# Performance work log

Measured on AMD Instinct MI355X. Metric: run time of the kernel, lower is better.

The kernel has to match this reference:

```python
import jax, jax.numpy as jnp
import numpy as np

NEG_SLOPE = 0.2  # PyG GATConv default leaky_relu slope


def gat_conv(x, ei, W, a_src, a_dst, b, heads, ch):
    """One PyG-style GATConv (eval mode, add_self_loops already applied to ei)."""
    N = x.shape[0]
    h = (x @ W).reshape(N, heads, ch)                      # [N,H,C]
    src, dst = ei[0], ei[1]
    al_s = jnp.sum(h * a_src, axis=-1)                     # [N,H]
    al_d = jnp.sum(h * a_dst, axis=-1)                     # [N,H]
    e = jax.nn.leaky_relu(al_s[src] + al_d[dst], NEG_SLOPE)  # [E,H]
    m = jax.ops.segment_max(e, dst, num_segments=N)        # stable softmax over in-edges
    ex = jnp.exp(e - m[dst])
    den = jax.ops.segment_sum(ex, dst, num_segments=N)
    alpha = ex / den[dst]                                  # [E,H]
    msg = alpha[:, :, None] * h[src]                       # [E,H,C]
    out = jax.ops.segment_sum(msg, dst, num_segments=N)    # [N,H,C]
    return out.reshape(N, heads * ch) + b


def setup_inputs() -> dict:
    key = jax.random.key(0)
    ks = jax.random.split(key, 12)
    N, E, D_in, C, H, D_out = 10000, 320000, 256, 128, 4, 64
    HC = H * C

    def glorot(k, shape):
        fan = shape[0] + shape[-1]
        return jax.random.normal(k, shape, dtype=jnp.float32) * np.sqrt(2.0 / fan)

    x = jax.random.normal(ks[0], (N, D_in), dtype=jnp.float32)
    edge_index = jax.random.randint(ks[1], (2, E), 0, N, dtype=jnp.int64)
    return {
        "x": x,
        "edge_index": edge_index,
        "W1": glorot(ks[2], (D_in, HC)),
        "a_src1": glorot(ks[3], (H, C)),
        "a_dst1": glorot(ks[4], (H, C)),
        "b1": jnp.zeros((HC,), dtype=jnp.float32),
        "W2": glorot(ks[5], (HC, HC)),
        "a_src2": glorot(ks[6], (H, C)),
        "a_dst2": glorot(ks[7], (H, C)),
        "b2": jnp.zeros((HC,), dtype=jnp.float32),
        "W3": glorot(ks[8], (HC, D_out)),
        "a_src3": glorot(ks[9], (1, D_out)),
        "a_dst3": glorot(ks[10], (1, D_out)),
        "b3": jnp.zeros((D_out,), dtype=jnp.float32),
    }


def reference(x, edge_index, W1, a_src1, a_dst1, b1, W2, a_src2, a_dst2, b2,
              W3, a_src3, a_dst3, b3):
    N = x.shape[0]
    loops = jnp.arange(N, dtype=edge_index.dtype)
    ei = jnp.concatenate([edge_index, jnp.stack([loops, loops])], axis=1)
    H, C = a_src1.shape
    h = jax.nn.elu(gat_conv(x, ei, W1, a_src1, a_dst1, b1, H, C))
    h = jax.nn.elu(gat_conv(h, ei, W2, a_src2, a_dst2, b2, H, C))
    out = gat_conv(h, ei, W3, a_src3, a_dst3, b3, 1, a_src3.shape[1])
    return out
```

## Files before the change

kernel.cpp:

```cpp
#include <hip/hip_runtime.h>
#include <hip/hip_fp16.h>

typedef _Float16 f16x8 __attribute__((ext_vector_type(8)));
typedef float f32x4 __attribute__((ext_vector_type(4)));

__device__ __forceinline__ unsigned short f2h_bits(float f) {
    __half h = __float2half(f);
    return *reinterpret_cast<unsigned short*>(&h);
}
__device__ __forceinline__ float h2f_bits(unsigned short u) {
    __half h = *reinterpret_cast<__half*>(&u);
    return __half2float(h);
}

__device__ __forceinline__ void fma_mix_lo(float& acc, float a, unsigned hw) {
    asm("v_fma_mix_f32 %0, %1, %2, %0 op_sel_hi:[0,1,0]"
        : "+v"(acc) : "v"(a), "v"(hw));
}
__device__ __forceinline__ void fma_mix_hi(float& acc, float a, unsigned hw) {
    asm("v_fma_mix_f32 %0, %1, %2, %0 op_sel:[0,1,0] op_sel_hi:[0,1,0]"
        : "+v"(acc) : "v"(a), "v"(hw));
}

__device__ __forceinline__ float elu_fast(float v) {
    float e = __expf(v) - 1.f;
    return v > 0.f ? v : e;
}

__device__ __forceinline__ void gload_lds16(const void* g, void* l) {
    __builtin_amdgcn_global_load_lds(
        (const __attribute__((address_space(1))) unsigned int*)g,
        (__attribute__((address_space(3))) unsigned int*)l, 16, 0, 0);
}

__global__ void k_prep(const float* __restrict__ W1, unsigned short* __restrict__ W1T,
                       const float* __restrict__ W2, unsigned short* __restrict__ W2T,
                       const float* __restrict__ W3, unsigned short* __restrict__ W3T,
                       const float* __restrict__ x, unsigned short* __restrict__ xb,
                       int* __restrict__ csr, int Mcap,
                       const int* __restrict__ ei, int E, int* __restrict__ deg,
                       int DIN, int HC, int DOUT, int N)
{
    int i = blockIdx.x * blockDim.x + threadIdx.x;
    int n1 = DIN * HC;
    int n2 = n1 + HC * HC;
    int n3 = n2 + HC * DOUT;
    int n4 = n3 + N * DIN;
    int n5 = n4 + Mcap;
    int n6 = n5 + E;
    if (i < n1) {
        int k = i / HC, n = i - k * HC;
        W1T[n * DIN + k] = f2h_bits(W1[i]);
    } else if (i < n2) {
        int j = i - n1;
        int k = j / HC, n = j - k * HC;
        W2T[n * HC + k] = f2h_bits(W2[j]);
    } else if (i < n3) {
        int j = i - n2;
        int k = j / DOUT, n = j - k * DOUT;
        W3T[n * HC + k] = f2h_bits(W3[j]);
    } else if (i < n4) {
        int j = i - n3;
        xb[j] = f2h_bits(x[j]);
    } else if (i < n5) {
        csr[i - n4] = -1;
    } else if (i < n6) {
        atomicAdd(&deg[ei[E + (i - n5)]], 1);
    }
}

__global__ void k_scan(const int* __restrict__ deg, int* __restrict__ off,
                       int* __restrict__ cur, int N) {
    __shared__ int sums[1024];
    int t = threadIdx.x;
    int chunk = (N + 1023) >> 10;
    int lo = t * chunk;
    int hi = lo + chunk; if (hi > N) hi = N;
    if (lo > N) lo = N;
    int s = 0;
    for (int i = lo; i < hi; ++i) s += (deg[i] + 4) & ~3;
    sums[t] = s;
    __syncthreads();
    for (int dd = 1; dd < 1024; dd <<= 1) {
        int v = (t >= dd) ? sums[t - dd] : 0;
        __syncthreads();
        sums[t] += v;
        __syncthreads();
    }
    int run = sums[t] - s;
    for (int i = lo; i < hi; ++i) { off[i] = run; cur[i] = run; run += (deg[i] + 4) & ~3; }
    if (t == 1023) off[N] = run;
}
__global__ void k_fill(const int* __restrict__ ei, int E, int N,
                       int* cur, int* __restrict__ csr) {
    int i = blockIdx.x * blockDim.x + threadIdx.x;
    if (i < E) {
        int s = ei[i], d = ei[E + i];
        int pos = atomicAdd(&cur[d], 1);
        csr[pos] = s;
    } else if (i < E + N) {
        int nn = i - E;
        int pos = atomicAdd(&cur[nn], 1);
        csr[pos] = nn;
    }
}

template <bool OUTH, bool DOAL>
__global__ __launch_bounds__(256) void k_gemm(
    const unsigned short* __restrict__ A, const unsigned short* __restrict__ BT,
    void* __restrict__ D, int M, int K, int Nc, int tiles_n,
    const float* __restrict__ asrc, const float* __restrict__ adst,
    float* __restrict__ als, float* __restrict__ ald)
{
    int wid = blockIdx.x * (blockDim.x >> 6) + (threadIdx.x >> 6);
    int tiles_m = (M + 63) >> 6;
    if (wid >= tiles_m * tiles_n) return;
    int lane = threadIdx.x & 63;
    int tm = wid / tiles_n, tn = wid - tm * tiles_n;
    int m0 = tm << 6, n0 = tn << 6;
    int r = lane & 15, q = lane >> 4;

    const unsigned short* Arow[4];
    const unsigned short* Brow[4];
#pragma unroll
    for (int i = 0; i < 4; ++i) {
        int row = m0 + 16 * i + r; row = row < M ? row : M - 1;
        Arow[i] = A + (size_t)row * K + q * 8;
        Brow[i] = BT + (size_t)(n0 + 16 * i + r) * K + q * 8;
    }

    f32x4 acc[4][4] = {};
    f16x8 a[4], b[4], a2[4], b2[4];
#pragma unroll
    for (int i = 0; i < 4; ++i) {
        a[i] = *(const f16x8*)(Arow[i]);
        b[i] = *(const f16x8*)(Brow[i]);
    }
    for (int k0 = 0; k0 < K; k0 += 32) {
        int kn = k0 + 32;
        if (kn < K) {
#pragma unroll
            for (int i = 0; i < 4; ++i) {
                a2[i] = *(const f16x8*)(Arow[i] + kn);
                b2[i] = *(const f16x8*)(Brow[i] + kn);
            }
        }
#pragma unroll
        for (int i = 0; i < 4; ++i)
#pragma unroll
            for (int j = 0; j < 4; ++j)
                acc[i][j] = __builtin_amdgcn_mfma_f32_16x16x32_f16(a[i], b[j], acc[i][j], 0, 0, 0);
        if (kn < K) {
#pragma unroll
            for (int i = 0; i < 4; ++i) { a[i] = a2[i]; b[i] = b2[i]; }
        }
    }
#pragma unroll
    for (int i = 0; i < 4; ++i) {
        int rowb = m0 + 16 * i + q * 4;
#pragma unroll
        for (int rr = 0; rr < 4; ++rr) {
            int row = rowb + rr;
            if (row < M) {
#pragma unroll
                for (int j = 0; j < 4; ++j) {
                    int col = n0 + 16 * j + r;
                    if (OUTH)
                        ((unsigned short*)D)[(size_t)row * Nc + col] = f2h_bits(acc[i][j][rr]);
                    else
                        ((float*)D)[(size_t)row * Nc + col] = acc[i][j][rr];
                }
            }
        }
    }
    if (DOAL) {
        float asl[4], adl[4];
#pragma unroll
        for (int j = 0; j < 4; ++j) { asl[j] = asrc[16 * j + r]; adl[j] = adst[16 * j + r]; }
#pragma unroll
        for (int i = 0; i < 4; ++i) {
#pragma unroll
            for (int rr = 0; rr < 4; ++rr) {
                float s = 0.f, d = 0.f;
#pragma unroll
                for (int j = 0; j < 4; ++j) {
                    s += acc[i][j][rr] * asl[j];
                    d += acc[i][j][rr] * adl[j];
                }
#pragma unroll
                for (int dd = 1; dd < 16; dd <<= 1) {
                    s += __shfl_xor(s, dd);
                    d += __shfl_xor(d, dd);
                }
                int row = m0 + 16 * i + q * 4 + rr;
                if (r == 0 && row < M) { als[row] = s; ald[row] = d; }
            }
        }
    }
}

__global__ __launch_bounds__(256) void k_gemm_lds(
    const unsigned short* __restrict__ A, const unsigned short* __restrict__ BT,
    unsigned short* __restrict__ D, int M, int K, int Nc, int tiles_n)
{
    __shared__ unsigned short As[128 * 32];
    __shared__ unsigned short Bs[64 * 32];
    int tm = blockIdx.x / tiles_n, tn = blockIdx.x - tm * tiles_n;
    int m0 = tm << 7, n0 = tn << 6;
    int tid = threadIdx.x;
    int w = tid >> 6, lane = tid & 63;
    int wr = w >> 1, wc = w & 1;
    int r = lane & 15, q = lane >> 4;

    int lrow = lane >> 2;
    int lch = (lane & 3) * 8;
    int ga0 = m0 + w * 16 + lrow;       if (ga0 >= M) ga0 = M - 1;
    int ga1 = m0 + (w + 4) * 16 + lrow; if (ga1 >= M) ga1 = M - 1;
    const unsigned short* pa0 = A + (size_t)ga0 * K + lch;
    const unsigned short* pa1 = A + (size_t)ga1 * K + lch;
    const unsigned short* pb  = BT + (size_t)(n0 + w * 16 + lrow) * K + lch;
    unsigned short* lA0 = As + w * 512;
    unsigned short* lA1 = As + (w + 4) * 512;
    unsigned short* lB  = Bs + w * 512;

    const unsigned short* arp = As + (wr * 64 + r) * 32 + q * 8;
    const unsigned short* brp = Bs + (wc * 32 + r) * 32 + q * 8;

    f32x4 acc[4][2] = {};
    for (int k0 = 0; k0 < K; k0 += 32) {
        gload_lds16(pa0 + k0, lA0);
        gload_lds16(pa1 + k0, lA1);
        gload_lds16(pb + k0, lB);
        __syncthreads();
        f16x8 a[4], b[2];
#pragma unroll
        for (int i = 0; i < 4; ++i) a[i] = *(const f16x8*)(arp + i * 16 * 32);
#pragma unroll
        for (int j = 0; j < 2; ++j) b[j] = *(const f16x8*)(brp + j * 16 * 32);
#pragma unroll
        for (int i = 0; i < 4; ++i)
#pragma unroll
            for (int j = 0; j < 2; ++j)
                acc[i][j] = __builtin_amdgcn_mfma_f32_16x16x32_f16(a[i], b[j], acc[i][j], 0, 0, 0);
        __syncthreads();
    }
#pragma unroll
    for (int i = 0; i < 4; ++i) {
        int rowb = m0 + wr * 64 + 16 * i + q * 4;
#pragma unroll
        for (int rr = 0; rr < 4; ++rr) {
            int row = rowb + rr;
            if (row < M) {
#pragma unroll
                for (int j = 0; j < 2; ++j) {
                    int col = n0 + wc * 32 + 16 * j + r;
                    D[(size_t)row * Nc + col] = f2h_bits(acc[i][j][rr]);
                }
            }
        }
    }
}

template <int HCt, int Ht>
__global__ __launch_bounds__(256) void k_al(
    const unsigned short* __restrict__ h, const float* __restrict__ asrc,
    const float* __restrict__ adst,
    float* __restrict__ als, float* __restrict__ ald, int N)
{
    int wid = blockIdx.x * (blockDim.x >> 6) + (threadIdx.x >> 6);
    if (wid >= N) return;
    int lane = threadIdx.x & 63;
    const int CH = HCt / 64;
    const int Gs = 64 / Ht;
    float s = 0.f, d = 0.f;
    if constexpr (CH == 8) {
        const uint4* hr = (const uint4*)(h + (size_t)wid * HCt) + lane;
        uint4 hv = *hr;
        unsigned wds[4] = {hv.x, hv.y, hv.z, hv.w};
        const f32x4* as4 = (const f32x4*)(asrc + lane * 8);
        const f32x4* ad4 = (const f32x4*)(adst + lane * 8);
        f32x4 av0 = as4[0], av1 = as4[1], dv0 = ad4[0], dv1 = ad4[1];
#pragma unroll
        for (int wv = 0; wv < 4; ++wv) {
            float a0 = (wv < 2) ? av0[2 * wv] : av1[2 * (wv - 2)];
            float a1 = (wv < 2) ? av0[2 * wv + 1] : av1[2 * (wv - 2) + 1];
            float d0 = (wv < 2) ? dv0[2 * wv] : dv1[2 * (wv - 2)];
            float d1 = (wv < 2) ? dv0[2 * wv + 1] : dv1[2 * (wv - 2) + 1];
            fma_mix_lo(s, a0, wds[wv]); fma_mix_hi(s, a1, wds[wv]);
            fma_mix_lo(d, d0, wds[wv]); fma_mix_hi(d, d1, wds[wv]);
        }
    } else {
        float hv = h2f_bits(h[(size_t)wid * HCt + lane]);
        s = hv * asrc[lane];
        d = hv * adst[lane];
    }
#pragma unroll
    for (int dd = 1; dd < Gs; dd <<= 1) {
        s += __shfl_xor(s, dd);
        d += __shfl_xor(d, dd);
    }
    if ((lane & (Gs - 1)) == 0) {
        int hh = lane / Gs;
        als[wid * Ht + hh] = s;
        ald[wid * Ht + hh] = d;
    }
}

template <bool DOELU>
__global__ __launch_bounds__(256) void k_aggr4f(
    const unsigned short* __restrict__ h, const float* __restrict__ als,
    const float* __restrict__ ald,
    const int* __restrict__ off, const int* __restrict__ csr,
    const float* __restrict__ bias,
    unsigned short* __restrict__ outp, int N, int nodeBlocks)
{
    __shared__ float alpS[4][64];
    __shared__ int   csrS[4][64];
    int head = blockIdx.x / nodeBlocks;
    int nb = blockIdx.x - head * nodeBlocks;
    int wid = threadIdx.x >> 6;
    int n = nb * 4 + wid;
    if (n >= N) return;
    int lane = threadIdx.x & 63;
    int g = lane >> 4;
    int p = lane & 15;

    int off0 = off[n];
    int degp = off[n + 1] - off0;
    float aldh = ald[n * 4 + head];
    const char* hB = (const char*)h;
    const unsigned offp = (unsigned)(head * 256 + p * 16);

    float acc[8] = {};
    float den = 0.f;

    for (int base = 0; base < degp; base += 64) {
        float av = 0.f;
        int sc = 0;
        int e = base + lane;
        if (e < degp) {
            int s = csr[off0 + e];
            if (s >= 0) {
                sc = s;
                float l = als[(size_t)(unsigned)s * 4 + head] + aldh;
                l = l > 0.f ? l : 0.2f * l;
                av = __expf(l);
            }
        }
        alpS[wid][lane] = av;
        csrS[wid][lane] = sc;

        int qn = (degp - base) >> 2; if (qn > 16) qn = 16;
        for (int qq = g; qq < qn; qq += 4) {
            int4 cs = *(const int4*)&csrS[wid][qq * 4];
            f32x4 af = *(const f32x4*)&alpS[wid][qq * 4];
            uint4 h0 = *(const uint4*)(hB + (size_t)((((unsigned)cs.x) << 10) + offp));
            uint4 h1 = *(const uint4*)(hB + (size_t)((((unsigned)cs.y) << 10) + offp));
            uint4 h2 = *(const uint4*)(hB + (size_t)((((unsigned)cs.z) << 10) + offp));
            uint4 h3 = *(const uint4*)(hB + (size_t)((((unsigned)cs.w) << 10) + offp));
            den += (af[0] + af[1]) + (af[2] + af[3]);
            unsigned w0[4] = {h0.x, h0.y, h0.z, h0.w};
            unsigned w1[4] = {h1.x, h1.y, h1.z, h1.w};
            unsigned w2[4] = {h2.x, h2.y, h2.z, h2.w};
            unsigned w3[4] = {h3.x, h3.y, h3.z, h3.w};
#pragma unroll
            for (int wv = 0; wv < 4; ++wv) {
                fma_mix_lo(acc[2 * wv],     af[0], w0[wv]);
                fma_mix_hi(acc[2 * wv + 1], af[0], w0[wv]);
            }
#pragma unroll
            for (int wv = 0; wv < 4; ++wv) {
                fma_mix_lo(acc[2 * wv],     af[1], w1[wv]);
                fma_mix_hi(acc[2 * wv + 1], af[1], w1[wv]);
            }
#pragma unroll
            for (int wv = 0; wv < 4; ++wv) {
                fma_mix_lo(acc[2 * wv],     af[2], w2[wv]);
                fma_mix_hi(acc[2 * wv + 1], af[2], w2[wv]);
            }
#pragma unroll
            for (int wv = 0; wv < 4; ++wv) {
                fma_mix_lo(acc[2 * wv],     af[3], w3[wv]);
                fma_mix_hi(acc[2 * wv + 1], af[3], w3[wv]);
            }
        }
    }

    den += __shfl_xor(den, 16);
    den += __shfl_xor(den, 32);
#pragma unroll
    for (int j = 0; j < 8; ++j) {
        acc[j] += __shfl_xor(acc[j], 16);
        acc[j] += __shfl_xor(acc[j], 32);
    }

    if (g == 0) {
        float inv = 1.f / den;
        int cb = head * 128 + p * 8;
        unsigned ww[4];
#pragma unroll
        for (int wv = 0; wv < 4; ++wv) {
            float v0 = acc[2 * wv] * inv + bias[cb + 2 * wv];
            float v1 = acc[2 * wv + 1] * inv + bias[cb + 2 * wv + 1];
            if (DOELU) {
                v0 = elu_fast(v0);
                v1 = elu_fast(v1);
            }
            ww[wv] = (unsigned)f2h_bits(v0) | ((unsigned)f2h_bits(v1) << 16);
        }
        uint4 o; o.x = ww[0]; o.y = ww[1]; o.z = ww[2]; o.w = ww[3];
        *((uint4*)(outp + (size_t)n * 512 + cb)) = o;
    }
}

__global__ __launch_bounds__(256) void k_aggr1c(
    const unsigned short* __restrict__ h, const float* __restrict__ als,
    const float* __restrict__ aldv, const int* __restrict__ off,
    const int* __restrict__ csr, const float* __restrict__ bias,
    float* __restrict__ outp, int N)
{
    __shared__ float alpS[4][64];
    __shared__ int   csrS[4][64];
    int wid = threadIdx.x >> 6;
    int n = blockIdx.x * 4 + wid;
    if (n >= N) return;
    int lane = threadIdx.x & 63;
    int g = lane >> 4;
    int p = lane & 15;

    int off0 = off[n];
    int degp = off[n + 1] - off0;
    float aldh = aldv[n];
    const char* hB = (const char*)h;
    const unsigned offp = (unsigned)(p * 8);

    float acc[4] = {};
    float den = 0.f;

    for (int base = 0; base < degp; base += 64) {
        float av = 0.f;
        int sc = 0;
        int e = base + lane;
        if (e < degp) {
            int s = csr[off0 + e];
            if (s >= 0) {
                sc = s;
                float l = als[s] + aldh;
                l = l > 0.f ? l : 0.2f * l;
                av = __expf(l);
            }
        }
        alpS[wid][lane] = av;
        csrS[wid][lane] = sc;

        int qn = (degp - base) >> 2; if (qn > 16) qn = 16;
        for (int qq = g; qq < qn; qq += 4) {
            int4 cs = *(const int4*)&csrS[wid][qq * 4];
            f32x4 af = *(const f32x4*)&alpS[wid][qq * 4];
            uint2 h0 = *(const uint2*)(hB + (size_t)((((unsigned)cs.x) << 7) + offp));
            uint2 h1 = *(const uint2*)(hB + (size_t)((((unsigned)cs.y) << 7) + offp));
            uint2 h2 = *(const uint2*)(hB + (size_t)((((unsigned)cs.z) << 7) + offp));
            uint2 h3 = *(const uint2*)(hB + (size_t)((((unsigned)cs.w) << 7) + offp));
            den += (af[0] + af[1]) + (af[2] + af[3]);
            fma_mix_lo(acc[0], af[0], h0.x);
            fma_mix_hi(acc[1], af[0], h0.x);
            fma_mix_lo(acc[2], af[0], h0.y);
            fma_mix_hi(acc[3], af[0], h0.y);
            fma_mix_lo(acc[0], af[1], h1.x);
            fma_mix_hi(acc[1], af[1], h1.x);
            fma_mix_lo(acc[2], af[1], h1.y);
            fma_mix_hi(acc[3], af[1], h1.y);
            fma_mix_lo(acc[0], af[2], h2.x);
            fma_mix_hi(acc[1], af[2], h2.x);
            fma_mix_lo(acc[2], af[2], h2.y);
            fma_mix_hi(acc[3], af[2], h2.y);
            fma_mix_lo(acc[0], af[3], h3.x);
            fma_mix_hi(acc[1], af[3], h3.x);
            fma_mix_lo(acc[2], af[3], h3.y);
            fma_mix_hi(acc[3], af[3], h3.y);
        }
    }

    den += __shfl_xor(den, 16);
    den += __shfl_xor(den, 32);
#pragma unroll
    for (int j = 0; j < 4; ++j) {
        acc[j] += __shfl_xor(acc[j], 16);
        acc[j] += __shfl_xor(acc[j], 32);
    }
    if (g == 0) {
        float inv = 1.f / den;
        f32x4 o;
#pragma unroll
        for (int j = 0; j < 4; ++j)
            o[j] = acc[j] * inv + bias[p * 4 + j];
        *((f32x4*)(outp + (size_t)n * 64 + p * 4)) = o;
    }
}

extern "C" void kernel_launch(void* const* d_in, const int* in_sizes, int n_in,
                              void* d_out, int out_size, void* d_ws, size_t ws_size,
                              hipStream_t stream)
{
    const float* x   = (const float*)d_in[0];
    const int*   ei  = (const int*)d_in[1];
    const float* W1  = (const float*)d_in[2];
    const float* as1 = (const float*)d_in[3];
    const float* ad1 = (const float*)d_in[4];
    const float* b1  = (const float*)d_in[5];
    const float* W2  = (const float*)d_in[6];
    const float* as2 = (const float*)d_in[7];
    const float* ad2 = (const float*)d_in[8];
    const float* b2  = (const float*)d_in[9];
    const float* W3  = (const float*)d_in[10];
    const float* as3 = (const float*)d_in[11];
    const float* ad3 = (const float*)d_in[12];
    const float* b3  = (const float*)d_in[13];

    const int DIN = 256, HC = 512, DOUT = 64;
    int N = in_sizes[0] / DIN;
    int E = in_sizes[1] / 2;
    int Mcap = E + 4 * N;

    char* w = (char*)d_ws;
    auto alloc = [&](size_t bytes) -> char* {
        char* p = w;
        w += (bytes + 255) & ~(size_t)255;
        return p;
    };
    int* deg    = (int*)alloc((size_t)N * 4);
    int* cur    = (int*)alloc((size_t)N * 4);
    int* off    = (int*)alloc((size_t)(N + 1) * 4);
    int* csr    = (int*)alloc((size_t)Mcap * 4);
    unsigned short* W1T = (unsigned short*)alloc((size_t)HC * DIN * 2);
    unsigned short* W2T = (unsigned short*)alloc((size_t)HC * HC * 2);
    unsigned short* W3T = (unsigned short*)alloc((size_t)DOUT * HC * 2);
    unsigned short* xb  = (unsigned short*)alloc((size_t)N * DIN * 2);
    unsigned short* act = (unsigned short*)alloc((size_t)N * HC * 2);
    unsigned short* hb  = (unsigned short*)alloc((size_t)N * HC * 2);
    unsigned short* hb3 = (unsigned short*)alloc((size_t)N * DOUT * 2);
    float* als   = (float*)alloc((size_t)N * 4 * 4);
    float* ald   = (float*)alloc((size_t)N * 4 * 4);

    hipMemsetAsync(deg, 0, (size_t)N * 4, stream);
    int prep_total = DIN * HC + HC * HC + HC * DOUT + N * DIN + Mcap + E;
    k_prep<<<(prep_total + 255) / 256, 256, 0, stream>>>(
        W1, W1T, W2, W2T, W3, W3T, x, xb, csr, Mcap, ei, E, deg, DIN, HC, DOUT, N);
    k_scan<<<1, 1024, 0, stream>>>(deg, off, cur, N);
    k_fill<<<(E + N + 255) / 256, 256, 0, stream>>>(ei, E, N, cur, csr);

    int tiles_m = (N + 63) / 64;
    auto gemm_blocks = [&](int tn) { return (tiles_m * tn + 3) / 4; };
    int tm128 = (N + 127) / 128;
    int nwave_blocks = (N + 3) / 4;
    int nodeBlocks = (N + 3) / 4;

    k_gemm_lds<<<tm128 * (HC / 64), 256, 0, stream>>>(xb, W1T, hb, N, DIN, HC, HC / 64);
    k_al<512, 4><<<nwave_blocks, 256, 0, stream>>>(hb, as1, ad1, als, ald, N);
    k_aggr4f<true><<<4 * nodeBlocks, 256, 0, stream>>>(hb, als, ald, off, csr, b1, act, N, nodeBlocks);

    k_gemm_lds<<<tm128 * (HC / 64), 256, 0, stream>>>(act, W2T, hb, N, HC, HC, HC / 64);
    k_al<512, 4><<<nwave_blocks, 256, 0, stream>>>(hb, as2, ad2, als, ald, N);
    k_aggr4f<true><<<4 * nodeBlocks, 256, 0, stream>>>(hb, als, ald, off, csr, b2, act, N, nodeBlocks);

    k_gemm<true, true><<<gemm_blocks(1), 256, 0, stream>>>(
        act, W3T, hb3, N, HC, DOUT, 1, as3, ad3, als, ald);
    k_aggr1c<<<nwave_blocks, 256, 0, stream>>>(hb3, als, ald, off, csr, b3, (float*)d_out, N);
}
```

Before: 263.8 us.

## Fold attention vectors into extra GEMM columns and drop k_al kernels

Precomputes W·a_src and W·a_dst per head as eight extra columns appended to the transposed fp16 weights (padded to 64 columns). The GEMM gets one extra column tile whose accumulators are written directly as the attention logits, so the separate k_al kernel, which re-read the whole hidden matrix, is removed for layers 1 and 2. The cost is an extra tile of MMA work per row block, a few more prep threads, and logits computed from fp16-rounded folded weights rather than from rounded h, which changes numerics slightly.

```diff
diff --git a/kernel.cpp b/kernel.cpp
--- a/kernel.cpp
+++ b/kernel.cpp
@@ -39,6 +39,8 @@
                        const float* __restrict__ x, unsigned short* __restrict__ xb,
                        int* __restrict__ csr, int Mcap,
                        const int* __restrict__ ei, int E, int* __restrict__ deg,
+                       const float* __restrict__ as1, const float* __restrict__ ad1,
+                       const float* __restrict__ as2, const float* __restrict__ ad2,
                        int DIN, int HC, int DOUT, int N)
 {
     int i = blockIdx.x * blockDim.x + threadIdx.x;
@@ -48,6 +50,9 @@
     int n4 = n3 + N * DIN;
     int n5 = n4 + Mcap;
     int n6 = n5 + E;
+    int n7 = n6 + 8 * DIN;
+    int n8 = n7 + 8 * HC;
+    int n9 = n8 + 56 * DIN + 56 * HC;
     if (i < n1) {
         int k = i / HC, n = i - k * HC;
         W1T[n * DIN + k] = f2h_bits(W1[i]);
@@ -66,6 +71,28 @@
         csr[i - n4] = -1;
     } else if (i < n6) {
         atomicAdd(&deg[ei[E + (i - n5)]], 1);
+    } else if (i < n7) {
+        int j = i - n6;
+        int h8 = j / DIN, k = j - h8 * DIN;
+        int hh = h8 & 3;
+        const float* av = (h8 < 4 ? as1 : ad1) + hh * 128;
+        const float* wr = W1 + (size_t)k * HC + hh * 128;
+        float s = 0.f;
+        for (int c = 0; c < 128; ++c) s += wr[c] * av[c];
+        W1T[(size_t)(HC + h8) * DIN + k] = f2h_bits(s);
+    } else if (i < n8) {
+        int j = i - n7;
+        int h8 = j / HC, k = j - h8 * HC;
+        int hh = h8 & 3;
+        const float* av = (h8 < 4 ? as2 : ad2) + hh * 128;
+        const float* wr = W2 + (size_t)k * HC + hh * 128;
+        float s = 0.f;
+        for (int c = 0; c < 128; ++c) s += wr[c] * av[c];
+        W2T[(size_t)(HC + h8) * HC + k] = f2h_bits(s);
+    } else if (i < n9) {
+        int j = i - n8;
+        if (j < 56 * DIN) W1T[(size_t)(HC + 8) * DIN + j] = 0;
+        else              W2T[(size_t)(HC + 8) * HC + (j - 56 * DIN)] = 0;
     }
 }
 
@@ -201,7 +228,8 @@
 
 __global__ __launch_bounds__(256) void k_gemm_lds(
     const unsigned short* __restrict__ A, const unsigned short* __restrict__ BT,
-    unsigned short* __restrict__ D, int M, int K, int Nc, int tiles_n)
+    unsigned short* __restrict__ D, int M, int K, int Nc, int tiles_n,
+    float* __restrict__ als, float* __restrict__ ald)
 {
     __shared__ unsigned short As[128 * 32];
     __shared__ unsigned short Bs[64 * 32];
@@ -244,6 +272,20 @@
                 acc[i][j] = __builtin_amdgcn_mfma_f32_16x16x32_f16(a[i], b[j], acc[i][j], 0, 0, 0);
         __syncthreads();
     }
+    if (tn == tiles_n - 1) {
+        if (wc == 0 && r < 8) {
+            float* dst = (r < 4) ? als : ald;
+            int hh = r & 3;
+#pragma unroll
+            for (int i = 0; i < 4; ++i)
+#pragma unroll
+                for (int rr = 0; rr < 4; ++rr) {
+                    int row = m0 + wr * 64 + 16 * i + q * 4 + rr;
+                    if (row < M) dst[row * 4 + hh] = acc[i][0][rr];
+                }
+        }
+        return;
+    }
 #pragma unroll
     for (int i = 0; i < 4; ++i) {
         int rowb = m0 + wr * 64 + 16 * i + q * 4;
@@ -258,51 +300,6 @@
                 }
             }
         }
-    }
-}
-
-template <int HCt, int Ht>
-__global__ __launch_bounds__(256) void k_al(
-    const unsigned short* __restrict__ h, const float* __restrict__ asrc,
-    const float* __restrict__ adst,
-    float* __restrict__ als, float* __restrict__ ald, int N)
-{
-    int wid = blockIdx.x * (blockDim.x >> 6) + (threadIdx.x >> 6);
-    if (wid >= N) return;
-    int lane = threadIdx.x & 63;
-    const int CH = HCt / 64;
-    const int Gs = 64 / Ht;
-    float s = 0.f, d = 0.f;
-    if constexpr (CH == 8) {
-        const uint4* hr = (const uint4*)(h + (size_t)wid * HCt) + lane;
-        uint4 hv = *hr;
-        unsigned wds[4] = {hv.x, hv.y, hv.z, hv.w};
-        const f32x4* as4 = (const f32x4*)(asrc + lane * 8);
-        const f32x4* ad4 = (const f32x4*)(adst + lane * 8);
-        f32x4 av0 = as4[0], av1 = as4[1], dv0 = ad4[0], dv1 = ad4[1];
-#pragma unroll
-        for (int wv = 0; wv < 4; ++wv) {
-            float a0 = (wv < 2) ? av0[2 * wv] : av1[2 * (wv - 2)];
-            float a1 = (wv < 2) ? av0[2 * wv + 1] : av1[2 * (wv - 2) + 1];
-            float d0 = (wv < 2) ? dv0[2 * wv] : dv1[2 * (wv - 2)];
-            float d1 = (wv < 2) ? dv0[2 * wv + 1] : dv1[2 * (wv - 2) + 1];
-            fma_mix_lo(s, a0, wds[wv]); fma_mix_hi(s, a1, wds[wv]);
-            fma_mix_lo(d, d0, wds[wv]); fma_mix_hi(d, d1, wds[wv]);
-        }
-    } else {
-        float hv = h2f_bits(h[(size_t)wid * HCt + lane]);
-        s = hv * asrc[lane];
-        d = hv * adst[lane];
-    }
-#pragma unroll
-    for (int dd = 1; dd < Gs; dd <<= 1) {
-        s += __shfl_xor(s, dd);
-        d += __shfl_xor(d, dd);
-    }
-    if ((lane & (Gs - 1)) == 0) {
-        int hh = lane / Gs;
-        als[wid * Ht + hh] = s;
-        ald[wid * Ht + hh] = d;
     }
 }
 
@@ -518,6 +515,7 @@
     const float* b3  = (const float*)d_in[13];
 
     const int DIN = 256, HC = 512, DOUT = 64;
+    const int EXT = 64;
     int N = in_sizes[0] / DIN;
     int E = in_sizes[1] / 2;
     int Mcap = E + 4 * N;
@@ -532,8 +530,8 @@
     int* cur    = (int*)alloc((size_t)N * 4);
     int* off    = (int*)alloc((size_t)(N + 1) * 4);
     int* csr    = (int*)alloc((size_t)Mcap * 4);
-    unsigned short* W1T = (unsigned short*)alloc((size_t)HC * DIN * 2);
-    unsigned short* W2T = (unsigned short*)alloc((size_t)HC * HC * 2);
+    unsigned short* W1T = (unsigned short*)alloc((size_t)(HC + EXT) * DIN * 2);
+    unsigned short* W2T = (unsigned short*)alloc((size_t)(HC + EXT) * HC * 2);
     unsigned short* W3T = (unsigned short*)alloc((size_t)DOUT * HC * 2);
     unsigned short* xb  = (unsigned short*)alloc((size_t)N * DIN * 2);
     unsigned short* act = (unsigned short*)alloc((size_t)N * HC * 2);
@@ -543,24 +541,25 @@
     float* ald   = (float*)alloc((size_t)N * 4 * 4);
 
     hipMemsetAsync(deg, 0, (size_t)N * 4, stream);
-    int prep_total = DIN * HC + HC * HC + HC * DOUT + N * DIN + Mcap + E;
+    int prep_total = DIN * HC + HC * HC + HC * DOUT + N * DIN + Mcap + E
+                   + 8 * DIN + 8 * HC + 56 * DIN + 56 * HC;
     k_prep<<<(prep_total + 255) / 256, 256, 0, stream>>>(
-        W1, W1T, W2, W2T, W3, W3T, x, xb, csr, Mcap, ei, E, deg, DIN, HC, DOUT, N);
+        W1, W1T, W2, W2T, W3, W3T, x, xb, csr, Mcap, ei, E, deg,
+        as1, ad1, as2, ad2, DIN, HC, DOUT, N);
     k_scan<<<1, 1024, 0, stream>>>(deg, off, cur, N);
     k_fill<<<(E + N + 255) / 256, 256, 0, stream>>>(ei, E, N, cur, csr);
 
     int tiles_m = (N + 63) / 64;
     auto gemm_blocks = [&](int tn) { return (tiles_m * tn + 3) / 4; };
     int tm128 = (N + 127) / 128;
+    int tiles_n12 = HC / 64 + 1;
     int nwave_blocks = (N + 3) / 4;
     int nodeBlocks = (N + 3) / 4;
 
-    k_gemm_lds<<<tm128 * (HC / 64), 256, 0, stream>>>(xb, W1T, hb, N, DIN, HC, HC / 64);
-    k_al<512, 4><<<nwave_blocks, 256, 0, stream>>>(hb, as1, ad1, als, ald, N);
+    k_gemm_lds<<<tm128 * tiles_n12, 256, 0, stream>>>(xb, W1T, hb, N, DIN, HC, tiles_n12, als, ald);
     k_aggr4f<true><<<4 * nodeBlocks, 256, 0, stream>>>(hb, als, ald, off, csr, b1, act, N, nodeBlocks);
 
-    k_gemm_lds<<<tm128 * (HC / 64), 256, 0, stream>>>(act, W2T, hb, N, HC, HC, HC / 64);
-    k_al<512, 4><<<nwave_blocks, 256, 0, stream>>>(hb, as2, ad2, als, ald, N);
+    k_gemm_lds<<<tm128 * tiles_n12, 256, 0, stream>>>(act, W2T, hb, N, HC, HC, tiles_n12, als, ald);
     k_aggr4f<true><<<4 * nodeBlocks, 256, 0, stream>>>(hb, als, ald, off, csr, b2, act, N, nodeBlocks);
 
     k_gemm<true, true><<<gemm_blocks(1), 256, 0, stream>>>(
```

Measured after the change: 263.6 us. Within noise of the previous version (-0.1%).

## Fuse attention logit computation into GEMM epilogue and double-buffer LDS tiles

Applied to the files above, without the earlier changes.

The per-node attention logit kernel (k_al) is removed. Its dot products with a_src/a_dst are now done in the GEMM epilogue: shuffle reductions across the 16 lanes give partial sums, which are added into zeroed per-layer buffers with atomics, since each head spans two 64-column tiles. The GEMM LDS staging is also double-buffered, so the next k-slice loads while MFMAs run on the current one, and the first barrier per iteration is dropped. The costs are extra atomics, doubled LDS use per block, and a larger memset to zero the logit buffers; the float atomic accumulation order is nondeterministic.

```diff
diff --git a/kernel.cpp b/kernel.cpp
--- a/kernel.cpp
+++ b/kernel.cpp
@@ -201,10 +201,12 @@
 
 __global__ __launch_bounds__(256) void k_gemm_lds(
     const unsigned short* __restrict__ A, const unsigned short* __restrict__ BT,
-    unsigned short* __restrict__ D, int M, int K, int Nc, int tiles_n)
+    unsigned short* __restrict__ D, int M, int K, int Nc, int tiles_n,
+    const float* __restrict__ asrc, const float* __restrict__ adst,
+    float* __restrict__ als, float* __restrict__ ald)
 {
-    __shared__ unsigned short As[128 * 32];
-    __shared__ unsigned short Bs[64 * 32];
+    __shared__ unsigned short As[2][128 * 32];
+    __shared__ unsigned short Bs[2][64 * 32];
     int tm = blockIdx.x / tiles_n, tn = blockIdx.x - tm * tiles_n;
     int m0 = tm << 7, n0 = tn << 6;
     int tid = threadIdx.x;
@@ -219,19 +221,21 @@
     const unsigned short* pa0 = A + (size_t)ga0 * K + lch;
     const unsigned short* pa1 = A + (size_t)ga1 * K + lch;
     const unsigned short* pb  = BT + (size_t)(n0 + w * 16 + lrow) * K + lch;
-    unsigned short* lA0 = As + w * 512;
-    unsigned short* lA1 = As + (w + 4) * 512;
-    unsigned short* lB  = Bs + w * 512;
-
-    const unsigned short* arp = As + (wr * 64 + r) * 32 + q * 8;
-    const unsigned short* brp = Bs + (wc * 32 + r) * 32 + q * 8;
+
+    auto stage = [&](int buf, int k0) {
+        gload_lds16(pa0 + k0, &As[buf][w * 512]);
+        gload_lds16(pa1 + k0, &As[buf][(w + 4) * 512]);
+        gload_lds16(pb + k0, &Bs[buf][w * 512]);
+    };
 
     f32x4 acc[4][2] = {};
+    stage(0, 0);
+    __syncthreads();
+    int cur = 0;
     for (int k0 = 0; k0 < K; k0 += 32) {
-        gload_lds16(pa0 + k0, lA0);
-        gload_lds16(pa1 + k0, lA1);
-        gload_lds16(pb + k0, lB);
-        __syncthreads();
+        if (k0 + 32 < K) stage(cur ^ 1, k0 + 32);
+        const unsigned short* arp = &As[cur][(wr * 64 + r) * 32 + q * 8];
+        const unsigned short* brp = &Bs[cur][(wc * 32 + r) * 32 + q * 8];
         f16x8 a[4], b[2];
 #pragma unroll
         for (int i = 0; i < 4; ++i) a[i] = *(const f16x8*)(arp + i * 16 * 32);
@@ -243,7 +247,9 @@
             for (int j = 0; j < 2; ++j)
                 acc[i][j] = __builtin_amdgcn_mfma_f32_16x16x32_f16(a[i], b[j], acc[i][j], 0, 0, 0);
         __syncthreads();
-    }
+        cur ^= 1;
+    }
+
 #pragma unroll
     for (int i = 0; i < 4; ++i) {
         int rowb = m0 + wr * 64 + 16 * i + q * 4;
@@ -259,51 +265,27 @@
             }
         }
     }
-}
-
-template <int HCt, int Ht>
-__global__ __launch_bounds__(256) void k_al(
-    const unsigned short* __restrict__ h, const float* __restrict__ asrc,
-    const float* __restrict__ adst,
-    float* __restrict__ als, float* __restrict__ ald, int N)
-{
-    int wid = blockIdx.x * (blockDim.x >> 6) + (threadIdx.x >> 6);
-    if (wid >= N) return;
-    int lane = threadIdx.x & 63;
-    const int CH = HCt / 64;
-    const int Gs = 64 / Ht;
-    float s = 0.f, d = 0.f;
-    if constexpr (CH == 8) {
-        const uint4* hr = (const uint4*)(h + (size_t)wid * HCt) + lane;
-        uint4 hv = *hr;
-        unsigned wds[4] = {hv.x, hv.y, hv.z, hv.w};
-        const f32x4* as4 = (const f32x4*)(asrc + lane * 8);
-        const f32x4* ad4 = (const f32x4*)(adst + lane * 8);
-        f32x4 av0 = as4[0], av1 = as4[1], dv0 = ad4[0], dv1 = ad4[1];
-#pragma unroll
-        for (int wv = 0; wv < 4; ++wv) {
-            float a0 = (wv < 2) ? av0[2 * wv] : av1[2 * (wv - 2)];
-            float a1 = (wv < 2) ? av0[2 * wv + 1] : av1[2 * (wv - 2) + 1];
-            float d0 = (wv < 2) ? dv0[2 * wv] : dv1[2 * (wv - 2)];
-            float d1 = (wv < 2) ? dv0[2 * wv + 1] : dv1[2 * (wv - 2) + 1];
-            fma_mix_lo(s, a0, wds[wv]); fma_mix_hi(s, a1, wds[wv]);
-            fma_mix_lo(d, d0, wds[wv]); fma_mix_hi(d, d1, wds[wv]);
-        }
-    } else {
-        float hv = h2f_bits(h[(size_t)wid * HCt + lane]);
-        s = hv * asrc[lane];
-        d = hv * adst[lane];
-    }
-#pragma unroll
-    for (int dd = 1; dd < Gs; dd <<= 1) {
-        s += __shfl_xor(s, dd);
-        d += __shfl_xor(d, dd);
-    }
-    if ((lane & (Gs - 1)) == 0) {
-        int hh = lane / Gs;
-        als[wid * Ht + hh] = s;
-        ald[wid * Ht + hh] = d;
-    }
+    int head = n0 >> 7;
+    int cbase = head * 128 + (n0 & 127) + wc * 32 + r;
+    float asl0 = asrc[cbase], asl1 = asrc[cbase + 16];
+    float adl0 = adst[cbase], adl1 = adst[cbase + 16];
+#pragma unroll
+    for (int i = 0; i < 4; ++i)
+#pragma unroll
+        for (int rr = 0; rr < 4; ++rr) {
+            float s = acc[i][0][rr] * asl0 + acc[i][1][rr] * asl1;
+            float d = acc[i][0][rr] * adl0 + acc[i][1][rr] * adl1;
+#pragma unroll
+            for (int dd = 1; dd < 16; dd <<= 1) {
+                s += __shfl_xor(s, dd);
+                d += __shfl_xor(d, dd);
+            }
+            int row = m0 + wr * 64 + 16 * i + q * 4 + rr;
+            if (r == 0 && row < M) {
+                atomicAdd(&als[row * 4 + head], s);
+                atomicAdd(&ald[row * 4 + head], d);
+            }
+        }
 }
 
 template <bool DOELU>
@@ -529,6 +511,11 @@
         return p;
     };
     int* deg    = (int*)alloc((size_t)N * 4);
+    float* als1 = (float*)alloc((size_t)N * 4 * 4);
+    float* ald1 = (float*)alloc((size_t)N * 4 * 4);
+    float* als2 = (float*)alloc((size_t)N * 4 * 4);
+    float* ald2 = (float*)alloc((size_t)N * 4 * 4);
+    char* zend  = w;
     int* cur    = (int*)alloc((size_t)N * 4);
     int* off    = (int*)alloc((size_t)(N + 1) * 4);
     int* csr    = (int*)alloc((size_t)Mcap * 4);
@@ -539,10 +526,10 @@
     unsigned short* act = (unsigned short*)alloc((size_t)N * HC * 2);
     unsigned short* hb  = (unsigned short*)alloc((size_t)N * HC * 2);
     unsigned short* hb3 = (unsigned short*)alloc((size_t)N * DOUT * 2);
-    float* als   = (float*)alloc((size_t)N * 4 * 4);
-    float* ald   = (float*)alloc((size_t)N * 4 * 4);
-
-    hipMemsetAsync(deg, 0, (size_t)N * 4, stream);
+    float* als3 = (float*)alloc((size_t)N * 4);
+    float* ald3 = (float*)alloc((size_t)N * 4);
+
+    hipMemsetAsync(deg, 0, (size_t)(zend - (char*)deg), stream);
     int prep_total = DIN * HC + HC * HC + HC * DOUT + N * DIN + Mcap + E;
     k_prep<<<(prep_total + 255) / 256, 256, 0, stream>>>(
         W1, W1T, W2, W2T, W3, W3T, x, xb, csr, Mcap, ei, E, deg, DIN, HC, DOUT, N);
@@ -552,18 +539,19 @@
     int tiles_m = (N + 63) / 64;
     auto gemm_blocks = [&](int tn) { return (tiles_m * tn + 3) / 4; };
     int tm128 = (N + 127) / 128;
+    int tiles_n8 = HC / 64;
     int nwave_blocks = (N + 3) / 4;
     int nodeBlocks = (N + 3) / 4;
 
-    k_gemm_lds<<<tm128 * (HC / 64), 256, 0, stream>>>(xb, W1T, hb, N, DIN, HC, HC / 64);
-    k_al<512, 4><<<nwave_blocks, 256, 0, stream>>>(hb, as1, ad1, als, ald, N);
-    k_aggr4f<true><<<4 * nodeBlocks, 256, 0, stream>>>(hb, als, ald, off, csr, b1, act, N, nodeBlocks);
-
-    k_gemm_lds<<<tm128 * (HC / 64), 256, 0, stream>>>(act, W2T, hb, N, HC, HC, HC / 64);
-    k_al<512, 4><<<nwave_blocks, 256, 0, stream>>>(hb, as2, ad2, als, ald, N);
-    k_aggr4f<true><<<4 * nodeBlocks, 256, 0, stream>>>(hb, als, ald, off, csr, b2, act, N, nodeBlocks);
+    k_gemm_lds<<<tm128 * tiles_n8, 256, 0, stream>>>(
+        xb, W1T, hb, N, DIN, HC, tiles_n8, as1, ad1, als1, ald1);
+    k_aggr4f<true><<<4 * nodeBlocks, 256, 0, stream>>>(hb, als1, ald1, off, csr, b1, act, N, nodeBlocks);
+
+    k_gemm_lds<<<tm128 * tiles_n8, 256, 0, stream>>>(
+        act, W2T, hb, N, HC, HC, tiles_n8, as2, ad2, als2, ald2);
+    k_aggr4f<true><<<4 * nodeBlocks, 256, 0, stream>>>(hb, als2, ald2, off, csr, b2, act, N, nodeBlocks);
 
     k_gemm<true, true><<<gemm_blocks(1), 256, 0, stream>>>(
-        act, W3T, hb3, N, HC, DOUT, 1, as3, ad3, als, ald);
-    k_aggr1c<<<nwave_blocks, 256, 0, stream>>>(hb3, als, ald, off, csr, b3, (float*)d_out, N);
-}
+        act, W3T, hb3, N, HC, DOUT, 1, as3, ad3, als3, ald3);
+    k_aggr1c<<<nwave_blocks, 256, 0, stream>>>(hb3, als3, ald3, off, csr, b3, (float*)d_out, N);
+}
```

Result: slower. 294.2 us (+11.5%).
